# Kernel tuning notes

Measured on AMD Instinct MI355X. Metric: run time of the kernel, lower is better.

## Reference

```python
import jax, jax.numpy as jnp
import numpy as np

N_NODES = 100000
F_IN = 64
F_OUT = 64
SLOPE = 0.2


def setup_inputs() -> dict:
    key = jax.random.key(0)
    k1, k2, k3, k4 = jax.random.split(key, 4)
    input_matrix = jax.random.normal(k1, (N_NODES, F_IN), dtype=jnp.float32)
    edge_index = jax.random.randint(k2, (2, 1600000), 0, N_NODES, dtype=jnp.int64)
    # xavier-uniform-style params
    lim_w = float(np.sqrt(6.0 / (F_IN + F_OUT)))
    W = jax.random.uniform(k3, (F_IN, F_OUT), minval=-lim_w, maxval=lim_w, dtype=jnp.float32)
    lim_a = float(np.sqrt(6.0 / (2 * F_OUT + 1)))
    a = jax.random.uniform(k4, (2 * F_OUT,), minval=-lim_a, maxval=lim_a, dtype=jnp.float32)
    return {"input_matrix": input_matrix, "edge_index": edge_index, "W": W, "a": a}


def reference(input_matrix, edge_index, W, a):
    N = input_matrix.shape[0]
    # add self edges
    loops = jnp.arange(N, dtype=edge_index.dtype)
    src = jnp.concatenate([edge_index[0], loops])  # [E+N]
    dst = jnp.concatenate([edge_index[1], loops])  # [E+N]

    h = input_matrix @ W                      # [N, F_out]
    F = h.shape[1]
    h_src = h[src]                            # [E+N, F_out] gather
    h_dst = h[dst]                            # [E+N, F_out] gather
    # cat([h_src, h_dst], 1) @ a == h_src @ a[:F] + h_dst @ a[F:]
    alpha = h_src @ a[:F] + h_dst @ a[F:]     # [E+N]
    alpha = jnp.where(alpha >= 0, alpha, SLOPE * alpha)  # leaky relu
    alpha = jnp.exp(alpha)
    denom = jax.ops.segment_sum(alpha, src, num_segments=N)  # [N]
    alpha = alpha / denom[src]                # segment softmax over edges sharing src
    out = jax.ops.segment_sum(h_dst * alpha[:, None], src, num_segments=N)  # [N, F_out]
    return out
```

## Files before the change

kernel.cpp:

```cpp
#include <hip/hip_runtime.h>
#include <hip/hip_bf16.h>

#define F 64
#define SLOPE 0.2f
#define NB_SHIFT 8
#define BATCH 4096
#define HIST_BLOCKS 128

__device__ inline unsigned short f2bf(float f) {
    unsigned u = __float_as_uint(f);
    unsigned r = (u + 0x7FFFu + ((u >> 16) & 1u)) >> 16;
    return (unsigned short)r;
}

__global__ __launch_bounds__(256) void gat_gemm_hist(
    const float* __restrict__ X, const float* __restrict__ W,
    const float* __restrict__ a, unsigned short* __restrict__ hb,
    float* __restrict__ s1, float* __restrict__ s2, int N,
    const int* __restrict__ src, int* __restrict__ partialHist, int E,
    int gemmBlocks) {
    __shared__ __align__(16) char smem[51200];
    const int tid = threadIdx.x;

    if ((int)blockIdx.x >= gemmBlocks) {
        int hbid = blockIdx.x - gemmBlocks;
        int* lh = (int*)smem;
        for (int i = tid; i < 512; i += 256) lh[i] = 0;
        __syncthreads();
        for (int i = hbid * 256 + tid; i < E; i += HIST_BLOCKS * 256)
            atomicAdd(&lh[src[i] >> NB_SHIFT], 1);
        __syncthreads();
        for (int i = tid; i < 512; i += 256)
            partialHist[hbid * 512 + i] = lh[i];
        return;
    }

    float* XsT = (float*)smem;
    float* Wsm = (float*)(smem + 33792);
    const int base = blockIdx.x * 128;

#pragma unroll
    for (int l = 0; l < 8; ++l) {
        int flat = l * 256 + tid;
        int rr = flat >> 4;
        int qc = flat & 15;
        float4 v = make_float4(0.f, 0.f, 0.f, 0.f);
        if (base + rr < N) v = *(const float4*)&X[(size_t)(base + rr) * F + qc * 4];
        XsT[(qc * 4 + 0) * 132 + rr] = v.x;
        XsT[(qc * 4 + 1) * 132 + rr] = v.y;
        XsT[(qc * 4 + 2) * 132 + rr] = v.z;
        XsT[(qc * 4 + 3) * 132 + rr] = v.w;
    }
#pragma unroll
    for (int l = 0; l < 4; ++l) {
        int flat = l * 256 + tid;
        int k = flat >> 4;
        int qc = flat & 15;
        float4 v = *(const float4*)&W[k * F + qc * 4];
        *(float4*)&Wsm[k * 68 + qc * 4] = v;
    }
    __syncthreads();

    const int r0 = (tid >> 4) * 8;
    const int c0 = (tid & 15) * 4;

    float4 acc[8];
#pragma unroll
    for (int i = 0; i < 8; ++i) acc[i] = make_float4(0.f, 0.f, 0.f, 0.f);

#pragma unroll 8
    for (int k = 0; k < F; ++k) {
        float4 xa = *(float4*)&XsT[k * 132 + r0];
        float4 xb = *(float4*)&XsT[k * 132 + r0 + 4];
        float4 wv = *(float4*)&Wsm[k * 68 + c0];
        float xs[8] = {xa.x, xa.y, xa.z, xa.w, xb.x, xb.y, xb.z, xb.w};
#pragma unroll
        for (int i = 0; i < 8; ++i) {
            acc[i].x = fmaf(xs[i], wv.x, acc[i].x);
            acc[i].y = fmaf(xs[i], wv.y, acc[i].y);
            acc[i].z = fmaf(xs[i], wv.z, acc[i].z);
            acc[i].w = fmaf(xs[i], wv.w, acc[i].w);
        }
    }

#pragma unroll
    for (int i = 0; i < 8; ++i) {
        int r = base + r0 + i;
        if (r < N) {
            ushort4 hv;
            hv.x = f2bf(acc[i].x);
            hv.y = f2bf(acc[i].y);
            hv.z = f2bf(acc[i].z);
            hv.w = f2bf(acc[i].w);
            *(ushort4*)&hb[(size_t)r * F + c0] = hv;
        }
    }

    float4 a1 = *(const float4*)&a[c0];
    float4 a2 = *(const float4*)&a[F + c0];
    __syncthreads();
    float2* red = (float2*)Wsm;
    const int cg = tid & 15;
#pragma unroll
    for (int i = 0; i < 8; ++i) {
        float p = acc[i].x * a1.x + acc[i].y * a1.y + acc[i].z * a1.z + acc[i].w * a1.w;
        float q = acc[i].x * a2.x + acc[i].y * a2.y + acc[i].z * a2.z + acc[i].w * a2.w;
        red[cg * 128 + r0 + i] = make_float2(p, q);
    }
    __syncthreads();
    if (tid < 128) {
        float p = 0.f, q = 0.f;
#pragma unroll
        for (int g = 0; g < 16; ++g) {
            float2 t = red[g * 128 + tid];
            p += t.x;
            q += t.y;
        }
        int r = base + tid;
        if (r < N) {
            s1[r] = p;
            s2[r] = q;
        }
    }
}

__global__ __launch_bounds__(512) void gat_scan0(
    const int* __restrict__ partialHist, int* __restrict__ bucketBase,
    int* __restrict__ bucketCursor, int* __restrict__ rowptrN, int NB) {
    __shared__ int wsum[8];
    int tid = threadIdx.x, lane = tid & 63, wid = tid >> 6;
    int v = 0;
    for (int p = 0; p < HIST_BLOCKS; ++p)
        v += partialHist[p * 512 + tid];
    int x = v;
#pragma unroll
    for (int off = 1; off < 64; off <<= 1) {
        int y = __shfl_up(x, off, 64);
        if (lane >= off) x += y;
    }
    if (lane == 63) wsum[wid] = x;
    __syncthreads();
    int add = 0;
    for (int w = 0; w < 8; ++w)
        if (w < wid) add += wsum[w];
    int excl = add + x - v;
    if (tid < NB) {
        bucketBase[tid] = excl;
        bucketCursor[tid] = excl;
    }
    if (tid == NB - 1) {
        bucketBase[NB] = excl + v;
        rowptrN[0] = excl + v;
    }
}

__global__ __launch_bounds__(512) void gat_bin(
    const int* __restrict__ src, const int* __restrict__ dst,
    int* __restrict__ bucketCursor, unsigned* __restrict__ bucketData, int E) {
    __shared__ int hist[512], excl[512], gbase[512], cur[512];
    __shared__ int wsum[8];
    __shared__ int2 staged[BATCH];
    int tid = threadIdx.x, lane = tid & 63, wid = tid >> 6;
    int base = blockIdx.x * BATCH;
    int n = E - base;
    if (n > BATCH) n = BATCH;

    hist[tid] = 0;
    __syncthreads();

    int se[8], de[8];
#pragma unroll
    for (int j = 0; j < 8; ++j) {
        int i = base + j * 512 + tid;
        se[j] = -1;
        de[j] = 0;
        if (i < E) {
            se[j] = src[i];
            de[j] = dst[i];
            atomicAdd(&hist[se[j] >> NB_SHIFT], 1);
        }
    }
    __syncthreads();
    int v = hist[tid];
    int x = v;
#pragma unroll
    for (int off = 1; off < 64; off <<= 1) {
        int y = __shfl_up(x, off, 64);
        if (lane >= off) x += y;
    }
    if (lane == 63) wsum[wid] = x;
    __syncthreads();
    int add = 0;
    for (int w = 0; w < 8; ++w)
        if (w < wid) add += wsum[w];
    int ex = add + x - v;
    excl[tid] = ex;
    cur[tid] = ex;
    __syncthreads();
#pragma unroll
    for (int j = 0; j < 8; ++j) {
        if (se[j] >= 0) {
            int b = se[j] >> NB_SHIFT;
            int pos = atomicAdd(&cur[b], 1);
            staged[pos] = make_int2(se[j], de[j]);
        }
    }
    if (v > 0)
        gbase[tid] = atomicAdd(&bucketCursor[tid], v);
    __syncthreads();
    for (int i = tid; i < n; i += 512) {
        int2 p = staged[i];
        int b = p.x >> NB_SHIFT;
        bucketData[gbase[b] + (i - excl[b])] =
            ((unsigned)(p.x & 255) << 24) | (unsigned)p.y;
    }
}

__global__ __launch_bounds__(256) void gat_bucket(
    const int* __restrict__ bucketBase, const unsigned* __restrict__ bucketData,
    int* __restrict__ rowptr, int* __restrict__ sortedDst, int N) {
    __shared__ int cnt[256], cur[256];
    __shared__ int wsum[4];
    int b = blockIdx.x;
    int tid = threadIdx.x, lane = tid & 63, wid = tid >> 6;
    int beg = bucketBase[b];
    int end = bucketBase[b + 1];
    int node0 = b << NB_SHIFT;

    cnt[tid] = 0;
    __syncthreads();
    for (int i = beg + tid; i < end; i += 256)
        atomicAdd(&cnt[bucketData[i] >> 24], 1);
    __syncthreads();
    int v = cnt[tid];
    int x = v;
#pragma unroll
    for (int off = 1; off < 64; off <<= 1) {
        int y = __shfl_up(x, off, 64);
        if (lane >= off) x += y;
    }
    if (lane == 63) wsum[wid] = x;
    __syncthreads();
    int add = 0;
    for (int w = 0; w < 4; ++w)
        if (w < wid) add += wsum[w];
    int excl = add + x - v;
    int node = node0 + tid;
    if (node < N) rowptr[node] = beg + excl;
    cur[tid] = beg + excl;
    __syncthreads();
    for (int i = beg + tid; i < end; i += 256) {
        unsigned w = bucketData[i];
        int pos = atomicAdd(&cur[w >> 24], 1);
        sortedDst[pos] = (int)(w & 0xFFFFFFu);
    }
}

__global__ __launch_bounds__(256) void gat_aggregate(
    const int* __restrict__ rowptr,
    const int* __restrict__ sortedDst,
    const float* __restrict__ s1, const float* __restrict__ s2,
    const unsigned short* __restrict__ hb, float* __restrict__ out, int N) {
    int tid = threadIdx.x;
    int node = blockIdx.x * 32 + (tid >> 3);
    if (node >= N) return;
    const int fo = (tid & 7) * 8;

    int beg = rowptr[node];
    int end = rowptr[node + 1];
    float s1s = s1[node];
    float as = s1s + s2[node];
    as = (as >= 0.f) ? as : SLOPE * as;
    as = expf(as);

    float accA[8], accB[8];
    {
        uint4 hv = *(const uint4*)&hb[(size_t)node * F + fo];
        accA[0] = as * __uint_as_float(hv.x << 16);
        accA[1] = as * __uint_as_float(hv.x & 0xFFFF0000u);
        accA[2] = as * __uint_as_float(hv.y << 16);
        accA[3] = as * __uint_as_float(hv.y & 0xFFFF0000u);
        accA[4] = as * __uint_as_float(hv.z << 16);
        accA[5] = as * __uint_as_float(hv.z & 0xFFFF0000u);
        accA[6] = as * __uint_as_float(hv.w << 16);
        accA[7] = as * __uint_as_float(hv.w & 0xFFFF0000u);
    }
#pragma unroll
    for (int i = 0; i < 8; ++i) accB[i] = 0.f;

    float dsum = as;
    int e = beg;
    for (; e + 2 <= end; e += 2) {
        int d0 = sortedDst[e];
        int d1 = sortedDst[e + 1];
        float t0 = s1s + s2[d0];
        float t1 = s1s + s2[d1];
        t0 = (t0 >= 0.f) ? t0 : SLOPE * t0;
        t1 = (t1 >= 0.f) ? t1 : SLOPE * t1;
        float a0 = expf(t0);
        float a1 = expf(t1);
        dsum += a0 + a1;
        uint4 g0 = *(const uint4*)&hb[(size_t)d0 * F + fo];
        uint4 g1 = *(const uint4*)&hb[(size_t)d1 * F + fo];
        accA[0] = fmaf(a0, __uint_as_float(g0.x << 16), accA[0]);
        accA[1] = fmaf(a0, __uint_as_float(g0.x & 0xFFFF0000u), accA[1]);
        accA[2] = fmaf(a0, __uint_as_float(g0.y << 16), accA[2]);
        accA[3] = fmaf(a0, __uint_as_float(g0.y & 0xFFFF0000u), accA[3]);
        accA[4] = fmaf(a0, __uint_as_float(g0.z << 16), accA[4]);
        accA[5] = fmaf(a0, __uint_as_float(g0.z & 0xFFFF0000u), accA[5]);
        accA[6] = fmaf(a0, __uint_as_float(g0.w << 16), accA[6]);
        accA[7] = fmaf(a0, __uint_as_float(g0.w & 0xFFFF0000u), accA[7]);
        accB[0] = fmaf(a1, __uint_as_float(g1.x << 16), accB[0]);
        accB[1] = fmaf(a1, __uint_as_float(g1.x & 0xFFFF0000u), accB[1]);
        accB[2] = fmaf(a1, __uint_as_float(g1.y << 16), accB[2]);
        accB[3] = fmaf(a1, __uint_as_float(g1.y & 0xFFFF0000u), accB[3]);
        accB[4] = fmaf(a1, __uint_as_float(g1.z << 16), accB[4]);
        accB[5] = fmaf(a1, __uint_as_float(g1.z & 0xFFFF0000u), accB[5]);
        accB[6] = fmaf(a1, __uint_as_float(g1.w << 16), accB[6]);
        accB[7] = fmaf(a1, __uint_as_float(g1.w & 0xFFFF0000u), accB[7]);
    }
    if (e < end) {
        int d0 = sortedDst[e];
        float t0 = s1s + s2[d0];
        t0 = (t0 >= 0.f) ? t0 : SLOPE * t0;
        float a0 = expf(t0);
        dsum += a0;
        uint4 g0 = *(const uint4*)&hb[(size_t)d0 * F + fo];
        accA[0] = fmaf(a0, __uint_as_float(g0.x << 16), accA[0]);
        accA[1] = fmaf(a0, __uint_as_float(g0.x & 0xFFFF0000u), accA[1]);
        accA[2] = fmaf(a0, __uint_as_float(g0.y << 16), accA[2]);
        accA[3] = fmaf(a0, __uint_as_float(g0.y & 0xFFFF0000u), accA[3]);
        accA[4] = fmaf(a0, __uint_as_float(g0.z << 16), accA[4]);
        accA[5] = fmaf(a0, __uint_as_float(g0.z & 0xFFFF0000u), accA[5]);
        accA[6] = fmaf(a0, __uint_as_float(g0.w << 16), accA[6]);
        accA[7] = fmaf(a0, __uint_as_float(g0.w & 0xFFFF0000u), accA[7]);
    }

    float inv = 1.0f / dsum;
    float4 r0, r1;
    r0.x = (accA[0] + accB[0]) * inv;
    r0.y = (accA[1] + accB[1]) * inv;
    r0.z = (accA[2] + accB[2]) * inv;
    r0.w = (accA[3] + accB[3]) * inv;
    r1.x = (accA[4] + accB[4]) * inv;
    r1.y = (accA[5] + accB[5]) * inv;
    r1.z = (accA[6] + accB[6]) * inv;
    r1.w = (accA[7] + accB[7]) * inv;
    *(float4*)&out[(size_t)node * F + fo] = r0;
    *(float4*)&out[(size_t)node * F + fo + 4] = r1;
}

extern "C" void kernel_launch(void* const* d_in, const int* in_sizes, int n_in,
                              void* d_out, int out_size, void* d_ws, size_t ws_size,
                              hipStream_t stream) {
    const float* X = (const float*)d_in[0];
    const int* edge = (const int*)d_in[1];
    const float* W = (const float*)d_in[2];
    const float* a = (const float*)d_in[3];

    int N = in_sizes[0] / F;
    int E = in_sizes[1] / 2;
    int NB = (N + 255) >> NB_SHIFT;

    const int* src = edge;
    const int* dst = edge + E;

    unsigned* bucketData = (unsigned*)d_ws;
    unsigned short* hb = (unsigned short*)(bucketData + E);
    float* s1 = (float*)(hb + (size_t)N * F);
    float* s2 = s1 + N;
    int* partialHist = (int*)(s2 + N);
    int* bucketBase = partialHist + HIST_BLOCKS * 512;
    int* bucketCursor = bucketBase + 513;
    int* rowptr = bucketCursor + 512;
    int* sortedDst = rowptr + (N + 1);

    float* out = (float*)d_out;

    int gemmBlocks = (N + 127) / 128;
    gat_gemm_hist<<<gemmBlocks + HIST_BLOCKS, 256, 0, stream>>>(
        X, W, a, hb, s1, s2, N, src, partialHist, E, gemmBlocks);

    gat_scan0<<<1, 512, 0, stream>>>(partialHist, bucketBase, bucketCursor,
                                     rowptr + N, NB);

    int binBlocks = (E + BATCH - 1) / BATCH;
    gat_bin<<<binBlocks, 512, 0, stream>>>(src, dst, bucketCursor, bucketData, E);

    gat_bucket<<<NB, 256, 0, stream>>>(bucketBase, bucketData, rowptr,
                                       sortedDst, N);

    int aggBlocks = (N + 31) / 32;
    gat_aggregate<<<aggBlocks, 256, 0, stream>>>(rowptr, sortedDst,
                                                 s1, s2, hb, out, N);
}
```

Measured before the change: 105.9 us.

## Fuse per-bucket counting sort with aggregation, using 128-node buckets and LDS-held sorted edges

Merges the bucket sort kernel and the aggregation kernel into one. Each block sorts its 128-node bucket's edges into shared memory and then aggregates those nodes directly, so the global rowptr and sortedDst round trip goes away. Bucket width drops from 256 to 128 nodes so a bucket (about 2k edges) fits in a 6144-entry LDS buffer, with a slow scan fallback for buckets that overflow. The histogram is split out of the GEMM launch into its own kernel, which adds one launch. Each block now does more serial work (4 nodes per 8-lane group), and only about 780 blocks run, which may lower parallelism in the gather phase.

```diff
diff --git a/kernel.cpp b/kernel.cpp
--- a/kernel.cpp
+++ b/kernel.cpp
@@ -3,9 +3,12 @@
 
 #define F 64
 #define SLOPE 0.2f
-#define NB_SHIFT 8
+#define NB_SHIFT 7
+#define BMASK 127
+#define NBMAX 1024
 #define BATCH 4096
 #define HIST_BLOCKS 128
+#define MAXE 6144
 
 __device__ inline unsigned short f2bf(float f) {
     unsigned u = __float_as_uint(f);
@@ -13,30 +16,15 @@
     return (unsigned short)r;
 }
 
-__global__ __launch_bounds__(256) void gat_gemm_hist(
+__global__ __launch_bounds__(256) void gat_gemm(
     const float* __restrict__ X, const float* __restrict__ W,
     const float* __restrict__ a, unsigned short* __restrict__ hb,
-    float* __restrict__ s1, float* __restrict__ s2, int N,
-    const int* __restrict__ src, int* __restrict__ partialHist, int E,
-    int gemmBlocks) {
+    float* __restrict__ s1, float* __restrict__ s2, int N) {
     __shared__ __align__(16) char smem[51200];
-    const int tid = threadIdx.x;
-
-    if ((int)blockIdx.x >= gemmBlocks) {
-        int hbid = blockIdx.x - gemmBlocks;
-        int* lh = (int*)smem;
-        for (int i = tid; i < 512; i += 256) lh[i] = 0;
-        __syncthreads();
-        for (int i = hbid * 256 + tid; i < E; i += HIST_BLOCKS * 256)
-            atomicAdd(&lh[src[i] >> NB_SHIFT], 1);
-        __syncthreads();
-        for (int i = tid; i < 512; i += 256)
-            partialHist[hbid * 512 + i] = lh[i];
-        return;
-    }
-
     float* XsT = (float*)smem;
     float* Wsm = (float*)(smem + 33792);
+
+    const int tid = threadIdx.x;
     const int base = blockIdx.x * 128;
 
 #pragma unroll
@@ -124,15 +112,32 @@
     }
 }
 
+__global__ __launch_bounds__(256) void gat_histb(
+    const int* __restrict__ src, int* __restrict__ partialHist, int E) {
+    __shared__ int lh[NBMAX];
+    int tid = threadIdx.x;
+    for (int i = tid; i < NBMAX; i += 256) lh[i] = 0;
+    __syncthreads();
+    for (int i = blockIdx.x * 256 + tid; i < E; i += HIST_BLOCKS * 256)
+        atomicAdd(&lh[src[i] >> NB_SHIFT], 1);
+    __syncthreads();
+    for (int i = tid; i < NBMAX; i += 256)
+        partialHist[blockIdx.x * NBMAX + i] = lh[i];
+}
+
 __global__ __launch_bounds__(512) void gat_scan0(
     const int* __restrict__ partialHist, int* __restrict__ bucketBase,
-    int* __restrict__ bucketCursor, int* __restrict__ rowptrN, int NB) {
+    int* __restrict__ bucketCursor, int NB) {
     __shared__ int wsum[8];
     int tid = threadIdx.x, lane = tid & 63, wid = tid >> 6;
-    int v = 0;
-    for (int p = 0; p < HIST_BLOCKS; ++p)
-        v += partialHist[p * 512 + tid];
-    int x = v;
+    int i0 = 2 * tid, i1 = 2 * tid + 1;
+    int v0 = 0, v1 = 0;
+    for (int p = 0; p < HIST_BLOCKS; ++p) {
+        v0 += partialHist[p * NBMAX + i0];
+        v1 += partialHist[p * NBMAX + i1];
+    }
+    int pv = v0 + v1;
+    int x = pv;
 #pragma unroll
     for (int off = 1; off < 64; off <<= 1) {
         int y = __shfl_up(x, off, 64);
@@ -143,21 +148,23 @@
     int add = 0;
     for (int w = 0; w < 8; ++w)
         if (w < wid) add += wsum[w];
-    int excl = add + x - v;
-    if (tid < NB) {
-        bucketBase[tid] = excl;
-        bucketCursor[tid] = excl;
-    }
-    if (tid == NB - 1) {
-        bucketBase[NB] = excl + v;
-        rowptrN[0] = excl + v;
-    }
+    int ex = add + x - pv;
+    if (i0 < NB) {
+        bucketBase[i0] = ex;
+        bucketCursor[i0] = ex;
+    }
+    if (i1 < NB) {
+        bucketBase[i1] = ex + v0;
+        bucketCursor[i1] = ex + v0;
+    }
+    if (i0 == NB - 1) bucketBase[NB] = ex + v0;
+    if (i1 == NB - 1) bucketBase[NB] = ex + v0 + v1;
 }
 
 __global__ __launch_bounds__(512) void gat_bin(
     const int* __restrict__ src, const int* __restrict__ dst,
     int* __restrict__ bucketCursor, unsigned* __restrict__ bucketData, int E) {
-    __shared__ int hist[512], excl[512], gbase[512], cur[512];
+    __shared__ int hist[NBMAX], excl[NBMAX], gbase[NBMAX], cur[NBMAX];
     __shared__ int wsum[8];
     __shared__ int2 staged[BATCH];
     int tid = threadIdx.x, lane = tid & 63, wid = tid >> 6;
@@ -166,6 +173,7 @@
     if (n > BATCH) n = BATCH;
 
     hist[tid] = 0;
+    hist[tid + 512] = 0;
     __syncthreads();
 
     int se[8], de[8];
@@ -181,8 +189,9 @@
         }
     }
     __syncthreads();
-    int v = hist[tid];
-    int x = v;
+    int v0 = hist[2 * tid], v1 = hist[2 * tid + 1];
+    int pv = v0 + v1;
+    int x = pv;
 #pragma unroll
     for (int off = 1; off < 64; off <<= 1) {
         int y = __shfl_up(x, off, 64);
@@ -193,9 +202,11 @@
     int add = 0;
     for (int w = 0; w < 8; ++w)
         if (w < wid) add += wsum[w];
-    int ex = add + x - v;
-    excl[tid] = ex;
-    cur[tid] = ex;
+    int ex = add + x - pv;
+    excl[2 * tid] = ex;
+    excl[2 * tid + 1] = ex + v0;
+    cur[2 * tid] = ex;
+    cur[2 * tid + 1] = ex + v0;
     __syncthreads();
 #pragma unroll
     for (int j = 0; j < 8; ++j) {
@@ -205,149 +216,201 @@
             staged[pos] = make_int2(se[j], de[j]);
         }
     }
-    if (v > 0)
-        gbase[tid] = atomicAdd(&bucketCursor[tid], v);
+    if (v0 > 0) gbase[2 * tid] = atomicAdd(&bucketCursor[2 * tid], v0);
+    if (v1 > 0) gbase[2 * tid + 1] = atomicAdd(&bucketCursor[2 * tid + 1], v1);
     __syncthreads();
     for (int i = tid; i < n; i += 512) {
         int2 p = staged[i];
         int b = p.x >> NB_SHIFT;
         bucketData[gbase[b] + (i - excl[b])] =
-            ((unsigned)(p.x & 255) << 24) | (unsigned)p.y;
-    }
-}
-
-__global__ __launch_bounds__(256) void gat_bucket(
+            ((unsigned)(p.x & BMASK) << 24) | (unsigned)p.y;
+    }
+}
+
+__global__ __launch_bounds__(256) void gat_bucket_agg(
     const int* __restrict__ bucketBase, const unsigned* __restrict__ bucketData,
-    int* __restrict__ rowptr, int* __restrict__ sortedDst, int N) {
-    __shared__ int cnt[256], cur[256];
-    __shared__ int wsum[4];
-    int b = blockIdx.x;
-    int tid = threadIdx.x, lane = tid & 63, wid = tid >> 6;
-    int beg = bucketBase[b];
-    int end = bucketBase[b + 1];
-    int node0 = b << NB_SHIFT;
-
-    cnt[tid] = 0;
-    __syncthreads();
-    for (int i = beg + tid; i < end; i += 256)
-        atomicAdd(&cnt[bucketData[i] >> 24], 1);
-    __syncthreads();
-    int v = cnt[tid];
-    int x = v;
-#pragma unroll
-    for (int off = 1; off < 64; off <<= 1) {
-        int y = __shfl_up(x, off, 64);
-        if (lane >= off) x += y;
-    }
-    if (lane == 63) wsum[wid] = x;
-    __syncthreads();
-    int add = 0;
-    for (int w = 0; w < 4; ++w)
-        if (w < wid) add += wsum[w];
-    int excl = add + x - v;
-    int node = node0 + tid;
-    if (node < N) rowptr[node] = beg + excl;
-    cur[tid] = beg + excl;
-    __syncthreads();
-    for (int i = beg + tid; i < end; i += 256) {
-        unsigned w = bucketData[i];
-        int pos = atomicAdd(&cur[w >> 24], 1);
-        sortedDst[pos] = (int)(w & 0xFFFFFFu);
-    }
-}
-
-__global__ __launch_bounds__(256) void gat_aggregate(
-    const int* __restrict__ rowptr,
-    const int* __restrict__ sortedDst,
     const float* __restrict__ s1, const float* __restrict__ s2,
     const unsigned short* __restrict__ hb, float* __restrict__ out, int N) {
-    int tid = threadIdx.x;
-    int node = blockIdx.x * 32 + (tid >> 3);
-    if (node >= N) return;
+    __shared__ int cnt[128], cur[128], rptr[129];
+    __shared__ int wsum[4];
+    __shared__ int sortedDstL[MAXE];
+
+    const int b = blockIdx.x;
+    const int tid = threadIdx.x, lane = tid & 63, wid = tid >> 6;
+    const int node0 = b << NB_SHIFT;
+    const int beg = bucketBase[b];
+    const int end = bucketBase[b + 1];
+    const int n = end - beg;
+
     const int fo = (tid & 7) * 8;
-
-    int beg = rowptr[node];
-    int end = rowptr[node + 1];
-    float s1s = s1[node];
-    float as = s1s + s2[node];
-    as = (as >= 0.f) ? as : SLOPE * as;
-    as = expf(as);
-
-    float accA[8], accB[8];
-    {
-        uint4 hv = *(const uint4*)&hb[(size_t)node * F + fo];
-        accA[0] = as * __uint_as_float(hv.x << 16);
-        accA[1] = as * __uint_as_float(hv.x & 0xFFFF0000u);
-        accA[2] = as * __uint_as_float(hv.y << 16);
-        accA[3] = as * __uint_as_float(hv.y & 0xFFFF0000u);
-        accA[4] = as * __uint_as_float(hv.z << 16);
-        accA[5] = as * __uint_as_float(hv.z & 0xFFFF0000u);
-        accA[6] = as * __uint_as_float(hv.w << 16);
-        accA[7] = as * __uint_as_float(hv.w & 0xFFFF0000u);
-    }
-#pragma unroll
-    for (int i = 0; i < 8; ++i) accB[i] = 0.f;
-
-    float dsum = as;
-    int e = beg;
-    for (; e + 2 <= end; e += 2) {
-        int d0 = sortedDst[e];
-        int d1 = sortedDst[e + 1];
-        float t0 = s1s + s2[d0];
-        float t1 = s1s + s2[d1];
-        t0 = (t0 >= 0.f) ? t0 : SLOPE * t0;
-        t1 = (t1 >= 0.f) ? t1 : SLOPE * t1;
-        float a0 = expf(t0);
-        float a1 = expf(t1);
-        dsum += a0 + a1;
-        uint4 g0 = *(const uint4*)&hb[(size_t)d0 * F + fo];
-        uint4 g1 = *(const uint4*)&hb[(size_t)d1 * F + fo];
-        accA[0] = fmaf(a0, __uint_as_float(g0.x << 16), accA[0]);
-        accA[1] = fmaf(a0, __uint_as_float(g0.x & 0xFFFF0000u), accA[1]);
-        accA[2] = fmaf(a0, __uint_as_float(g0.y << 16), accA[2]);
-        accA[3] = fmaf(a0, __uint_as_float(g0.y & 0xFFFF0000u), accA[3]);
-        accA[4] = fmaf(a0, __uint_as_float(g0.z << 16), accA[4]);
-        accA[5] = fmaf(a0, __uint_as_float(g0.z & 0xFFFF0000u), accA[5]);
-        accA[6] = fmaf(a0, __uint_as_float(g0.w << 16), accA[6]);
-        accA[7] = fmaf(a0, __uint_as_float(g0.w & 0xFFFF0000u), accA[7]);
-        accB[0] = fmaf(a1, __uint_as_float(g1.x << 16), accB[0]);
-        accB[1] = fmaf(a1, __uint_as_float(g1.x & 0xFFFF0000u), accB[1]);
-        accB[2] = fmaf(a1, __uint_as_float(g1.y << 16), accB[2]);
-        accB[3] = fmaf(a1, __uint_as_float(g1.y & 0xFFFF0000u), accB[3]);
-        accB[4] = fmaf(a1, __uint_as_float(g1.z << 16), accB[4]);
-        accB[5] = fmaf(a1, __uint_as_float(g1.z & 0xFFFF0000u), accB[5]);
-        accB[6] = fmaf(a1, __uint_as_float(g1.w << 16), accB[6]);
-        accB[7] = fmaf(a1, __uint_as_float(g1.w & 0xFFFF0000u), accB[7]);
-    }
-    if (e < end) {
-        int d0 = sortedDst[e];
-        float t0 = s1s + s2[d0];
-        t0 = (t0 >= 0.f) ? t0 : SLOPE * t0;
-        float a0 = expf(t0);
-        dsum += a0;
-        uint4 g0 = *(const uint4*)&hb[(size_t)d0 * F + fo];
-        accA[0] = fmaf(a0, __uint_as_float(g0.x << 16), accA[0]);
-        accA[1] = fmaf(a0, __uint_as_float(g0.x & 0xFFFF0000u), accA[1]);
-        accA[2] = fmaf(a0, __uint_as_float(g0.y << 16), accA[2]);
-        accA[3] = fmaf(a0, __uint_as_float(g0.y & 0xFFFF0000u), accA[3]);
-        accA[4] = fmaf(a0, __uint_as_float(g0.z << 16), accA[4]);
-        accA[5] = fmaf(a0, __uint_as_float(g0.z & 0xFFFF0000u), accA[5]);
-        accA[6] = fmaf(a0, __uint_as_float(g0.w << 16), accA[6]);
-        accA[7] = fmaf(a0, __uint_as_float(g0.w & 0xFFFF0000u), accA[7]);
-    }
-
-    float inv = 1.0f / dsum;
-    float4 r0, r1;
-    r0.x = (accA[0] + accB[0]) * inv;
-    r0.y = (accA[1] + accB[1]) * inv;
-    r0.z = (accA[2] + accB[2]) * inv;
-    r0.w = (accA[3] + accB[3]) * inv;
-    r1.x = (accA[4] + accB[4]) * inv;
-    r1.y = (accA[5] + accB[5]) * inv;
-    r1.z = (accA[6] + accB[6]) * inv;
-    r1.w = (accA[7] + accB[7]) * inv;
-    *(float4*)&out[(size_t)node * F + fo] = r0;
-    *(float4*)&out[(size_t)node * F + fo + 4] = r1;
+    const int sgId = tid >> 3;
+
+    if (n <= MAXE) {
+        if (tid < 128) cnt[tid] = 0;
+        __syncthreads();
+        for (int i = beg + tid; i < end; i += 256)
+            atomicAdd(&cnt[bucketData[i] >> 24], 1);
+        __syncthreads();
+        int v = (tid < 128) ? cnt[tid] : 0;
+        int x = v;
+#pragma unroll
+        for (int off = 1; off < 64; off <<= 1) {
+            int y = __shfl_up(x, off, 64);
+            if (lane >= off) x += y;
+        }
+        if (lane == 63) wsum[wid] = x;
+        __syncthreads();
+        int add = 0;
+        for (int w = 0; w < 4; ++w)
+            if (w < wid) add += wsum[w];
+        int excl = add + x - v;
+        if (tid < 128) {
+            rptr[tid] = excl;
+            cur[tid] = excl;
+        }
+        if (tid == 127) rptr[128] = excl + v;
+        __syncthreads();
+        for (int i = beg + tid; i < end; i += 256) {
+            unsigned w = bucketData[i];
+            int pos = atomicAdd(&cur[w >> 24], 1);
+            sortedDstL[pos] = (int)(w & 0xFFFFFFu);
+        }
+        __syncthreads();
+
+#pragma unroll
+        for (int it = 0; it < 4; ++it) {
+            int r = sgId * 4 + it;
+            int node = node0 + r;
+            if (node >= N) continue;
+            int eb = rptr[r], ee = rptr[r + 1];
+            float s1s = s1[node];
+            float as = s1s + s2[node];
+            as = (as >= 0.f) ? as : SLOPE * as;
+            as = expf(as);
+
+            float accA[8], accB[8];
+            {
+                uint4 hv = *(const uint4*)&hb[(size_t)node * F + fo];
+                accA[0] = as * __uint_as_float(hv.x << 16);
+                accA[1] = as * __uint_as_float(hv.x & 0xFFFF0000u);
+                accA[2] = as * __uint_as_float(hv.y << 16);
+                accA[3] = as * __uint_as_float(hv.y & 0xFFFF0000u);
+                accA[4] = as * __uint_as_float(hv.z << 16);
+                accA[5] = as * __uint_as_float(hv.z & 0xFFFF0000u);
+                accA[6] = as * __uint_as_float(hv.w << 16);
+                accA[7] = as * __uint_as_float(hv.w & 0xFFFF0000u);
+            }
+#pragma unroll
+            for (int i = 0; i < 8; ++i) accB[i] = 0.f;
+
+            float dsum = as;
+            int e = eb;
+            for (; e + 2 <= ee; e += 2) {
+                int d0 = sortedDstL[e];
+                int d1 = sortedDstL[e + 1];
+                float t0 = s1s + s2[d0];
+                float t1 = s1s + s2[d1];
+                t0 = (t0 >= 0.f) ? t0 : SLOPE * t0;
+                t1 = (t1 >= 0.f) ? t1 : SLOPE * t1;
+                float a0 = expf(t0);
+                float a1 = expf(t1);
+                dsum += a0 + a1;
+                uint4 g0 = *(const uint4*)&hb[(size_t)d0 * F + fo];
+                uint4 g1 = *(const uint4*)&hb[(size_t)d1 * F + fo];
+                accA[0] = fmaf(a0, __uint_as_float(g0.x << 16), accA[0]);
+                accA[1] = fmaf(a0, __uint_as_float(g0.x & 0xFFFF0000u), accA[1]);
+                accA[2] = fmaf(a0, __uint_as_float(g0.y << 16), accA[2]);
+                accA[3] = fmaf(a0, __uint_as_float(g0.y & 0xFFFF0000u), accA[3]);
+                accA[4] = fmaf(a0, __uint_as_float(g0.z << 16), accA[4]);
+                accA[5] = fmaf(a0, __uint_as_float(g0.z & 0xFFFF0000u), accA[5]);
+                accA[6] = fmaf(a0, __uint_as_float(g0.w << 16), accA[6]);
+                accA[7] = fmaf(a0, __uint_as_float(g0.w & 0xFFFF0000u), accA[7]);
+                accB[0] = fmaf(a1, __uint_as_float(g1.x << 16), accB[0]);
+                accB[1] = fmaf(a1, __uint_as_float(g1.x & 0xFFFF0000u), accB[1]);
+                accB[2] = fmaf(a1, __uint_as_float(g1.y << 16), accB[2]);
+                accB[3] = fmaf(a1, __uint_as_float(g1.y & 0xFFFF0000u), accB[3]);
+                accB[4] = fmaf(a1, __uint_as_float(g1.z << 16), accB[4]);
+                accB[5] = fmaf(a1, __uint_as_float(g1.z & 0xFFFF0000u), accB[5]);
+                accB[6] = fmaf(a1, __uint_as_float(g1.w << 16), accB[6]);
+                accB[7] = fmaf(a1, __uint_as_float(g1.w & 0xFFFF0000u), accB[7]);
+            }
+            if (e < ee) {
+                int d0 = sortedDstL[e];
+                float t0 = s1s + s2[d0];
+                t0 = (t0 >= 0.f) ? t0 : SLOPE * t0;
+                float a0 = expf(t0);
+                dsum += a0;
+                uint4 g0 = *(const uint4*)&hb[(size_t)d0 * F + fo];
+                accA[0] = fmaf(a0, __uint_as_float(g0.x << 16), accA[0]);
+                accA[1] = fmaf(a0, __uint_as_float(g0.x & 0xFFFF0000u), accA[1]);
+                accA[2] = fmaf(a0, __uint_as_float(g0.y << 16), accA[2]);
+                accA[3] = fmaf(a0, __uint_as_float(g0.y & 0xFFFF0000u), accA[3]);
+                accA[4] = fmaf(a0, __uint_as_float(g0.z << 16), accA[4]);
+                accA[5] = fmaf(a0, __uint_as_float(g0.z & 0xFFFF0000u), accA[5]);
+                accA[6] = fmaf(a0, __uint_as_float(g0.w << 16), accA[6]);
+                accA[7] = fmaf(a0, __uint_as_float(g0.w & 0xFFFF0000u), accA[7]);
+            }
+
+            float inv = 1.0f / dsum;
+            float4 r0v, r1v;
+            r0v.x = (accA[0] + accB[0]) * inv;
+            r0v.y = (accA[1] + accB[1]) * inv;
+            r0v.z = (accA[2] + accB[2]) * inv;
+            r0v.w = (accA[3] + accB[3]) * inv;
+            r1v.x = (accA[4] + accB[4]) * inv;
+            r1v.y = (accA[5] + accB[5]) * inv;
+            r1v.z = (accA[6] + accB[6]) * inv;
+            r1v.w = (accA[7] + accB[7]) * inv;
+            *(float4*)&out[(size_t)node * F + fo] = r0v;
+            *(float4*)&out[(size_t)node * F + fo + 4] = r1v;
+        }
+    } else {
+        for (int it = 0; it < 4; ++it) {
+            int r = sgId * 4 + it;
+            int node = node0 + r;
+            if (node >= N) continue;
+            float s1s = s1[node];
+            float as = s1s + s2[node];
+            as = (as >= 0.f) ? as : SLOPE * as;
+            as = expf(as);
+            float acc[8];
+            {
+                uint4 hv = *(const uint4*)&hb[(size_t)node * F + fo];
+                acc[0] = as * __uint_as_float(hv.x << 16);
+                acc[1] = as * __uint_as_float(hv.x & 0xFFFF0000u);
+                acc[2] = as * __uint_as_float(hv.y << 16);
+                acc[3] = as * __uint_as_float(hv.y & 0xFFFF0000u);
+                acc[4] = as * __uint_as_float(hv.z << 16);
+                acc[5] = as * __uint_as_float(hv.z & 0xFFFF0000u);
+                acc[6] = as * __uint_as_float(hv.w << 16);
+                acc[7] = as * __uint_as_float(hv.w & 0xFFFF0000u);
+            }
+            float dsum = as;
+            for (int i = beg; i < end; ++i) {
+                unsigned w = bucketData[i];
+                if ((int)(w >> 24) != r) continue;
+                int d0 = (int)(w & 0xFFFFFFu);
+                float t0 = s1s + s2[d0];
+                t0 = (t0 >= 0.f) ? t0 : SLOPE * t0;
+                float a0 = expf(t0);
+                dsum += a0;
+                uint4 g0 = *(const uint4*)&hb[(size_t)d0 * F + fo];
+                acc[0] = fmaf(a0, __uint_as_float(g0.x << 16), acc[0]);
+                acc[1] = fmaf(a0, __uint_as_float(g0.x & 0xFFFF0000u), acc[1]);
+                acc[2] = fmaf(a0, __uint_as_float(g0.y << 16), acc[2]);
+                acc[3] = fmaf(a0, __uint_as_float(g0.y & 0xFFFF0000u), acc[3]);
+                acc[4] = fmaf(a0, __uint_as_float(g0.z << 16), acc[4]);
+                acc[5] = fmaf(a0, __uint_as_float(g0.z & 0xFFFF0000u), acc[5]);
+                acc[6] = fmaf(a0, __uint_as_float(g0.w << 16), acc[6]);
+                acc[7] = fmaf(a0, __uint_as_float(g0.w & 0xFFFF0000u), acc[7]);
+            }
+            float inv = 1.0f / dsum;
+            float4 r0v = make_float4(acc[0] * inv, acc[1] * inv, acc[2] * inv, acc[3] * inv);
+            float4 r1v = make_float4(acc[4] * inv, acc[5] * inv, acc[6] * inv, acc[7] * inv);
+            *(float4*)&out[(size_t)node * F + fo] = r0v;
+            *(float4*)&out[(size_t)node * F + fo + 4] = r1v;
+        }
+    }
 }
 
 extern "C" void kernel_launch(void* const* d_in, const int* in_sizes, int n_in,
@@ -360,7 +423,7 @@
 
     int N = in_sizes[0] / F;
     int E = in_sizes[1] / 2;
-    int NB = (N + 255) >> NB_SHIFT;
+    int NB = (N + BMASK) >> NB_SHIFT;
 
     const int* src = edge;
     const int* dst = edge + E;
@@ -370,27 +433,21 @@
     float* s1 = (float*)(hb + (size_t)N * F);
     float* s2 = s1 + N;
     int* partialHist = (int*)(s2 + N);
-    int* bucketBase = partialHist + HIST_BLOCKS * 512;
-    int* bucketCursor = bucketBase + 513;
-    int* rowptr = bucketCursor + 512;
-    int* sortedDst = rowptr + (N + 1);
+    int* bucketBase = partialHist + HIST_BLOCKS * NBMAX;
+    int* bucketCursor = bucketBase + (NBMAX + 1);
 
     float* out = (float*)d_out;
 
     int gemmBlocks = (N + 127) / 128;
-    gat_gemm_hist<<<gemmBlocks + HIST_BLOCKS, 256, 0, stream>>>(
-        X, W, a, hb, s1, s2, N, src, partialHist, E, gemmBlocks);
-
-    gat_scan0<<<1, 512, 0, stream>>>(partialHist, bucketBase, bucketCursor,
-                                     rowptr + N, NB);
+    gat_gemm<<<gemmBlocks, 256, 0, stream>>>(X, W, a, hb, s1, s2, N);
+
+    gat_histb<<<HIST_BLOCKS, 256, 0, stream>>>(src, partialHist, E);
+
+    gat_scan0<<<1, 512, 0, stream>>>(partialHist, bucketBase, bucketCursor, NB);
 
     int binBlocks = (E + BATCH - 1) / BATCH;
     gat_bin<<<binBlocks, 512, 0, stream>>>(src, dst, bucketCursor, bucketData, E);
 
-    gat_bucket<<<NB, 256, 0, stream>>>(bucketBase, bucketData, rowptr,
-                                       sortedDst, N);
-
-    int aggBlocks = (N + 31) / 32;
-    gat_aggregate<<<aggBlocks, 256, 0, stream>>>(rowptr, sortedDst,
-                                                 s1, s2, hb, out, N);
-}
+    gat_bucket_agg<<<NB, 256, 0, stream>>>(bucketBase, bucketData, s1, s2, hb,
+                                           out, N);
+}
```

New measurement: 126.6 us. 1.2x slower.
